# Performance work log

Measured on AMD Instinct MI355X. Metric: run time of the kernel, lower is better.

## Reference

```python
import jax, jax.numpy as jnp
import numpy as np

B, SQ, SD, H = 64, 64, 512, 128


def setup_inputs() -> dict:
    key = jax.random.key(0)
    k1, k2, k3, k4, k5 = jax.random.split(key, 5)
    q = jax.random.normal(k1, (B, SQ, H), dtype=jnp.float32)
    d_pos = jax.random.normal(k2, (B, SD, H), dtype=jnp.float32)
    d_neg = jax.random.normal(k3, (B, SD, H), dtype=jnp.float32)
    mask_pos = jax.random.randint(k4, (B, SD), 0, 2, dtype=jnp.int32).at[:, 0].set(1)
    mask_neg = jax.random.randint(k5, (B, SD), 0, 2, dtype=jnp.int32).at[:, 0].set(1)
    return {"q": q, "d_pos": d_pos, "d_neg": d_neg,
            "mask_pos": mask_pos, "mask_neg": mask_neg}


def _colbert_maxsim(q, d, mask):
    # q: [a, s, h], d: [b, t, h], mask: [b, t] -> scores [a, b]
    simis = jnp.einsum('ash,bth->abst', q, d)            # [a, b, s, t]
    simis = jnp.where(mask[None, :, None, :] == 0, -jnp.inf, simis)
    return simis.max(axis=3).sum(axis=2)                 # max over t, sum over s


def reference(q, d_pos, d_neg, mask_pos, mask_neg):
    # Concatenate pos and in-batch-negative score blocks -> [B, 2B]
    distances = jnp.concatenate(
        [_colbert_maxsim(q, d_pos, mask_pos),
         _colbert_maxsim(q, d_neg, mask_neg)], axis=1)
    labels = jnp.arange(q.shape[0])
    logp = jax.nn.log_softmax(distances, axis=1)
    loss = -jnp.take_along_axis(logp, labels[:, None], axis=1).mean()
    return loss
```

## Files before the change

### kernel.cpp

```cpp
#include <hip/hip_runtime.h>
#include <hip/hip_bf16.h>
#include <math.h>
#include <stdint.h>

#define BB 64
#define SQN 64
#define SDN 512
#define HH 128

typedef __attribute__((ext_vector_type(8))) short bf16x8;
typedef __attribute__((ext_vector_type(16))) float f32x16;

__device__ __forceinline__ short f2bf(float f) {
  union { float f; unsigned u; } x; x.f = f;
  unsigned r = x.u + 0x7fffu + ((x.u >> 16) & 1u);
  return (short)(r >> 16);
}

__device__ __forceinline__ void gl_lds16(const short* g, short* l) {
  __builtin_amdgcn_global_load_lds(
      (const __attribute__((address_space(1))) unsigned int*)g,
      (__attribute__((address_space(3))) unsigned int*)l, 16, 0, 0);
}

__global__ __launch_bounds__(64)
void compact_meta(const int* __restrict__ mp, const int* __restrict__ mn,
                  int* __restrict__ perm, int* __restrict__ nchunks) {
  const int b = blockIdx.x, side = blockIdx.y;
  const int* mask = side ? mn : mp;
  const int ln = threadIdx.x;
  const int base = (side * BB + b) * SDN;
  int run = 0;
  #pragma unroll
  for (int it = 0; it < SDN / 64; ++it) {
    int t = it * 64 + ln;
    int m = mask[b * SDN + t];
    unsigned long long bal = __ballot(m != 0);
    int pos = run + __popcll(bal & ((1ull << ln) - 1ull));
    if (m) perm[base + pos] = t;
    run += (int)__popcll(bal);
  }
  int pad = (run + 127) & ~127;
  for (int j = run + ln; j < pad; j += 64) perm[base + j] = -1;
  if (ln == 0) nchunks[side * BB + b] = pad >> 7;
}

__global__ __launch_bounds__(256)
void convert_all(const float* __restrict__ q, const float* __restrict__ dp,
                 const float* __restrict__ dn, const int* __restrict__ perm,
                 short* __restrict__ oq, short* __restrict__ od) {
  const int D_BLOCKS = (2 * BB * SDN) / 8;
  if (blockIdx.x < D_BLOCKS) {
    int gid = blockIdx.x * 8 + (threadIdx.x >> 5);
    int l32 = threadIdx.x & 31;
    int bs = gid >> 9;
    int j  = gid & 511;
    int side = bs >> 6, b = bs & 63;
    int src_t = perm[bs * SDN + j];
    const float* srcmat = side ? dn : dp;
    float4 v = make_float4(0.f, 0.f, 0.f, 0.f);
    if (src_t >= 0)
      v = ((const float4*)(srcmat + ((size_t)b * SDN + src_t) * HH))[l32];
    short4 o; o.x = f2bf(v.x); o.y = f2bf(v.y); o.z = f2bf(v.z); o.w = f2bf(v.w);
    *(short4*)&od[((size_t)bs * SDN + j) * HH + l32 * 4] = o;
  } else {
    int i = (blockIdx.x - D_BLOCKS) * 256 + threadIdx.x;
    float4 v = ((const float4*)q)[i];
    short4 o; o.x = f2bf(v.x); o.y = f2bf(v.y); o.z = f2bf(v.z); o.w = f2bf(v.w);
    *(short4*)&oq[i * 4] = o;
  }
}

__global__ __launch_bounds__(256, 2)
void maxsim_kernel(const short* __restrict__ qb,
                   const short* __restrict__ dc,
                   const int* __restrict__ nchunks,
                   float* __restrict__ scores) {
  const int aslc = blockIdx.x;
  const int bs0  = blockIdx.y * 4;

  __shared__ __align__(16) short d_lds[2][128 * 128];

  const int tid = threadIdx.x;
  const int ln  = tid & 63;
  const int w   = tid >> 6;
  const int l31 = ln & 31;
  const int kh  = ln >> 5;
  const int a   = aslc * 4 + w;

  int nchv[4];
  #pragma unroll
  for (int i = 0; i < 4; ++i) nchv[i] = nchunks[bs0 + i];

  bf16x8 qfrag[2][8];
  #pragma unroll
  for (int half = 0; half < 2; ++half) {
    const short* qrow = qb + ((size_t)a * SQN + half * 32 + l31) * HH + kh * 8;
    #pragma unroll
    for (int kc = 0; kc < 8; ++kc)
      qfrag[half][kc] = *(const bf16x8*)(qrow + kc * 16);
  }

  float rmaxh[2] = {0.f, 0.f};

  {
    const short* dsrc = dc + (size_t)bs0 * SDN * HH;
    #pragma unroll
    for (int it = 0; it < 8; ++it) {
      int f = it * 256 + tid;
      int row = f >> 4;
      int c = (f & 15) ^ (row & 15);
      gl_lds16(&dsrc[row * HH + c * 8], &d_lds[0][(it * 256 + w * 64) * 8]);
    }
  }
  __syncthreads();

  int bi = 0, tc = 0, buf = 0;
  for (;;) {
    int nbi = bi, ntc = tc + 1;
    if (ntc == nchv[bi]) { ntc = 0; nbi = bi + 1; }
    const bool hn = (nbi < 4);

    if (hn) {
      const short* dsrc = dc + ((size_t)(bs0 + nbi) * SDN + ntc * 128) * HH;
      short* dst = &d_lds[buf ^ 1][0];
      #pragma unroll
      for (int it = 0; it < 8; ++it) {
        int f = it * 256 + tid;
        int row = f >> 4;
        int c = (f & 15) ^ (row & 15);
        gl_lds16(&dsrc[row * HH + c * 8], &dst[(it * 256 + w * 64) * 8]);
      }
    }

    const short* bufp = &d_lds[buf][0];
    #pragma unroll
    for (int tt = 0; tt < 4; ++tt) {
      int trow = tt * 32 + l31;
      int tm = trow & 15;
      const short* bbase = &bufp[trow * HH];
      f32x16 acc0 = {0,0,0,0,0,0,0,0,0,0,0,0,0,0,0,0};
      f32x16 acc1 = {0,0,0,0,0,0,0,0,0,0,0,0,0,0,0,0};
      #pragma unroll
      for (int kc = 0; kc < 8; ++kc) {
        int c = (kc * 2 + kh) ^ tm;
        bf16x8 dfrag = *(const bf16x8*)&bbase[c * 8];
        acc0 = __builtin_amdgcn_mfma_f32_32x32x16_bf16(dfrag, qfrag[0][kc], acc0, 0, 0, 0);
        acc1 = __builtin_amdgcn_mfma_f32_32x32x16_bf16(dfrag, qfrag[1][kc], acc1, 0, 0, 0);
      }
      float m0 = acc0[0], m1 = acc1[0];
      #pragma unroll
      for (int r = 1; r < 16; ++r) {
        m0 = fmaxf(m0, acc0[r]);
        m1 = fmaxf(m1, acc1[r]);
      }
      rmaxh[0] = fmaxf(rmaxh[0], m0);
      rmaxh[1] = fmaxf(rmaxh[1], m1);
    }

    if (ntc == 0) {
      float v0 = fmaxf(rmaxh[0], __shfl_xor(rmaxh[0], 32));
      float v1 = fmaxf(rmaxh[1], __shfl_xor(rmaxh[1], 32));
      float s = v0 + v1;
      s += __shfl_xor(s, 1);  s += __shfl_xor(s, 2);  s += __shfl_xor(s, 4);
      s += __shfl_xor(s, 8);  s += __shfl_xor(s, 16);
      if (ln == 0) scores[(size_t)a * (2 * BB) + bs0 + bi] = s;
      rmaxh[0] = 0.f; rmaxh[1] = 0.f;
    }

    __syncthreads();
    if (!hn) break;
    bi = nbi; tc = ntc; buf ^= 1;
  }
}

__global__ __launch_bounds__(1024)
void loss_kernel(const float* __restrict__ scores, float* __restrict__ out) {
  __shared__ float part[16];
  const int tid = threadIdx.x;
  const int ln = tid & 63;
  const int w  = tid >> 6;
  float acc = 0.f;
  #pragma unroll
  for (int i = 0; i < 4; ++i) {
    int r = w * 4 + i;
    float v0 = scores[r * 128 + ln];
    float v1 = scores[r * 128 + 64 + ln];
    float mx = fmaxf(v0, v1);
    #pragma unroll
    for (int off = 32; off >= 1; off >>= 1) mx = fmaxf(mx, __shfl_xor(mx, off));
    float e = __expf(v0 - mx) + __expf(v1 - mx);
    #pragma unroll
    for (int off = 32; off >= 1; off >>= 1) e += __shfl_xor(e, off);
    float lse = mx + __logf(e);
    float diag = __shfl(v0, r);
    acc += lse - diag;
  }
  if (ln == 0) part[w] = acc;
  __syncthreads();
  if (w == 0) {
    float v = (ln < 16) ? part[ln] : 0.f;
    #pragma unroll
    for (int off = 8; off >= 1; off >>= 1) v += __shfl_xor(v, off);
    if (ln == 0) out[0] = v * (1.0f / 64.0f);
  }
}

extern "C" void kernel_launch(void* const* d_in, const int* in_sizes, int n_in,
                              void* d_out, int out_size, void* d_ws, size_t ws_size,
                              hipStream_t stream) {
  const float* q        = (const float*)d_in[0];
  const float* d_pos    = (const float*)d_in[1];
  const float* d_neg    = (const float*)d_in[2];
  const int*   mask_pos = (const int*)d_in[3];
  const int*   mask_neg = (const int*)d_in[4];

  short* q_bf = (short*)d_ws;
  short* d_c  = q_bf + (size_t)BB * SQN * HH;
  int*   perm = (int*)(d_c + (size_t)2 * BB * SDN * HH);
  int*   nchunks = perm + 2 * BB * SDN;
  float* scores  = (float*)(nchunks + 128);

  compact_meta<<<dim3(BB, 2), 64, 0, stream>>>(mask_pos, mask_neg, perm, nchunks);

  const int D_BLOCKS = (2 * BB * SDN) / 8;
  const int Q_BLOCKS = (BB * SQN * HH / 4) / 256;
  convert_all<<<D_BLOCKS + Q_BLOCKS, 256, 0, stream>>>(q, d_pos, d_neg, perm,
                                                       q_bf, d_c);

  dim3 grid(16 , 32 );
  maxsim_kernel<<<grid, 256, 0, stream>>>(q_bf, d_c, nchunks, scores);

  loss_kernel<<<1, 1024, 0, stream>>>(scores, (float*)d_out);
}
```

Measured before the change: 131.8 us.

## Skip padded rows in conversion and tail tiles in maxsim, remap blocks per XCD

Records the valid-row count per document set and uses it to skip converting rows beyond the padded chunk range. It also skips MFMA tiles past the last valid row in each final chunk. Blocks are remapped so those sharing the same document sets are grouped on the same XCD, to improve L2 reuse. The skip adds a data-dependent branch and extra metadata loads.

```diff
diff --git a/kernel.cpp b/kernel.cpp
--- a/kernel.cpp
+++ b/kernel.cpp
@@ -25,7 +25,8 @@
 
 __global__ __launch_bounds__(64)
 void compact_meta(const int* __restrict__ mp, const int* __restrict__ mn,
-                  int* __restrict__ perm, int* __restrict__ nchunks) {
+                  int* __restrict__ perm, int* __restrict__ nchunks,
+                  int* __restrict__ nvalid) {
   const int b = blockIdx.x, side = blockIdx.y;
   const int* mask = side ? mn : mp;
   const int ln = threadIdx.x;
@@ -42,12 +43,16 @@
   }
   int pad = (run + 127) & ~127;
   for (int j = run + ln; j < pad; j += 64) perm[base + j] = -1;
-  if (ln == 0) nchunks[side * BB + b] = pad >> 7;
+  if (ln == 0) {
+    nchunks[side * BB + b] = pad >> 7;
+    nvalid[side * BB + b]  = run;
+  }
 }
 
 __global__ __launch_bounds__(256)
 void convert_all(const float* __restrict__ q, const float* __restrict__ dp,
                  const float* __restrict__ dn, const int* __restrict__ perm,
+                 const int* __restrict__ nchunks,
                  short* __restrict__ oq, short* __restrict__ od) {
   const int D_BLOCKS = (2 * BB * SDN) / 8;
   if (blockIdx.x < D_BLOCKS) {
@@ -55,6 +60,7 @@
     int l32 = threadIdx.x & 31;
     int bs = gid >> 9;
     int j  = gid & 511;
+    if (j >= (nchunks[bs] << 7)) return;
     int side = bs >> 6, b = bs & 63;
     int src_t = perm[bs * SDN + j];
     const float* srcmat = side ? dn : dp;
@@ -75,9 +81,13 @@
 void maxsim_kernel(const short* __restrict__ qb,
                    const short* __restrict__ dc,
                    const int* __restrict__ nchunks,
+                   const int* __restrict__ nvalid,
                    float* __restrict__ scores) {
-  const int aslc = blockIdx.x;
-  const int bs0  = blockIdx.y * 4;
+  const int lid  = blockIdx.x + 16 * blockIdx.y;
+  const int xcd  = lid & 7;
+  const int slot = lid >> 3;
+  const int aslc = slot & 15;
+  const int bs0  = (xcd + 8 * (slot >> 4)) * 4;
 
   __shared__ __align__(16) short d_lds[2][128 * 128];
 
@@ -88,9 +98,12 @@
   const int kh  = ln >> 5;
   const int a   = aslc * 4 + w;
 
-  int nchv[4];
-  #pragma unroll
-  for (int i = 0; i < 4; ++i) nchv[i] = nchunks[bs0 + i];
+  int nchv[4], nvv[4];
+  #pragma unroll
+  for (int i = 0; i < 4; ++i) {
+    nchv[i] = nchunks[bs0 + i];
+    nvv[i]  = nvalid[bs0 + i];
+  }
 
   bf16x8 qfrag[2][8];
   #pragma unroll
@@ -133,29 +146,34 @@
       }
     }
 
+    const int ntt = (tc == nchv[bi] - 1)
+                        ? ((nvv[bi] - (tc << 7) + 31) >> 5)
+                        : 4;
     const short* bufp = &d_lds[buf][0];
     #pragma unroll
     for (int tt = 0; tt < 4; ++tt) {
-      int trow = tt * 32 + l31;
-      int tm = trow & 15;
-      const short* bbase = &bufp[trow * HH];
-      f32x16 acc0 = {0,0,0,0,0,0,0,0,0,0,0,0,0,0,0,0};
-      f32x16 acc1 = {0,0,0,0,0,0,0,0,0,0,0,0,0,0,0,0};
-      #pragma unroll
-      for (int kc = 0; kc < 8; ++kc) {
-        int c = (kc * 2 + kh) ^ tm;
-        bf16x8 dfrag = *(const bf16x8*)&bbase[c * 8];
-        acc0 = __builtin_amdgcn_mfma_f32_32x32x16_bf16(dfrag, qfrag[0][kc], acc0, 0, 0, 0);
-        acc1 = __builtin_amdgcn_mfma_f32_32x32x16_bf16(dfrag, qfrag[1][kc], acc1, 0, 0, 0);
+      if (tt < ntt) {
+        int trow = tt * 32 + l31;
+        int tm = trow & 15;
+        const short* bbase = &bufp[trow * HH];
+        f32x16 acc0 = {0,0,0,0,0,0,0,0,0,0,0,0,0,0,0,0};
+        f32x16 acc1 = {0,0,0,0,0,0,0,0,0,0,0,0,0,0,0,0};
+        #pragma unroll
+        for (int kc = 0; kc < 8; ++kc) {
+          int c = (kc * 2 + kh) ^ tm;
+          bf16x8 dfrag = *(const bf16x8*)&bbase[c * 8];
+          acc0 = __builtin_amdgcn_mfma_f32_32x32x16_bf16(dfrag, qfrag[0][kc], acc0, 0, 0, 0);
+          acc1 = __builtin_amdgcn_mfma_f32_32x32x16_bf16(dfrag, qfrag[1][kc], acc1, 0, 0, 0);
+        }
+        float m0 = acc0[0], m1 = acc1[0];
+        #pragma unroll
+        for (int r = 1; r < 16; ++r) {
+          m0 = fmaxf(m0, acc0[r]);
+          m1 = fmaxf(m1, acc1[r]);
+        }
+        rmaxh[0] = fmaxf(rmaxh[0], m0);
+        rmaxh[1] = fmaxf(rmaxh[1], m1);
       }
-      float m0 = acc0[0], m1 = acc1[0];
-      #pragma unroll
-      for (int r = 1; r < 16; ++r) {
-        m0 = fmaxf(m0, acc0[r]);
-        m1 = fmaxf(m1, acc1[r]);
-      }
-      rmaxh[0] = fmaxf(rmaxh[0], m0);
-      rmaxh[1] = fmaxf(rmaxh[1], m1);
     }
 
     if (ntc == 0) {
@@ -219,17 +237,19 @@
   short* d_c  = q_bf + (size_t)BB * SQN * HH;
   int*   perm = (int*)(d_c + (size_t)2 * BB * SDN * HH);
   int*   nchunks = perm + 2 * BB * SDN;
-  float* scores  = (float*)(nchunks + 128);
-
-  compact_meta<<<dim3(BB, 2), 64, 0, stream>>>(mask_pos, mask_neg, perm, nchunks);
+  int*   nvalid  = nchunks + 128;
+  float* scores  = (float*)(nvalid + 128);
+
+  compact_meta<<<dim3(BB, 2), 64, 0, stream>>>(mask_pos, mask_neg, perm,
+                                               nchunks, nvalid);
 
   const int D_BLOCKS = (2 * BB * SDN) / 8;
   const int Q_BLOCKS = (BB * SQN * HH / 4) / 256;
   convert_all<<<D_BLOCKS + Q_BLOCKS, 256, 0, stream>>>(q, d_pos, d_neg, perm,
-                                                       q_bf, d_c);
+                                                       nchunks, q_bf, d_c);
 
   dim3 grid(16 , 32 );
-  maxsim_kernel<<<grid, 256, 0, stream>>>(q_bf, d_c, nchunks, scores);
+  maxsim_kernel<<<grid, 256, 0, stream>>>(q_bf, d_c, nchunks, nvalid, scores);
 
   loss_kernel<<<1, 1024, 0, stream>>>(scores, (float*)d_out);
 }
```

New measurement: 126.5 us. 1.04x faster.
